# Optimization experiments

Measured on AMD Instinct MI355X. Metric: run time of the kernel, lower is better.

## Reference

```python
import jax, jax.numpy as jnp
import numpy as np

# -------- problem dimensions (match init_kwargs / input_specs) --------
B, N, D = 4, 16384, 64          # batch, nodes (=128*128 pixels), feature dim
Q = 128                         # plateau/propagation state width (hardcoded in forward)
W = H = 128                     # grid (hardcoded in forward)
E = 131072                      # edges per batch element
M = 4                           # num_masks = k_nodes - 1
NUM_ITERS = 25                  # GraphPropagator(num_iters=25)
ADJ_THRESH = 0.5                # GraphPropagator(adj_thresh=0.5)


def setup_inputs() -> dict:
    key = jax.random.key(0)
    k1, k2, k3, k4 = jax.random.split(key, 4)
    node_features = jax.random.normal(k1, (B, N, D), dtype=jnp.float32)
    # global node indices in [0, B*N) -- the torch code concatenates per-batch
    # edge lists directly into a (B*N, B*N) SparseTensor
    node_edges = jax.random.randint(k2, (B, 2, E), 0, B * N)
    node_weights = jax.random.uniform(k3, (B, E), dtype=jnp.float32)
    init_state = jax.random.normal(k4, (B, N, Q), dtype=jnp.float32)
    return {"node_features": node_features, "node_edges": node_edges,
            "node_weights": node_weights, "init_state": init_state}


def _propagate(init_state, rows, cols, ws):
    """25-iteration sparse label propagation on the global (B*N,B*N) graph."""
    h = init_state.reshape(B * N, Q)

    def step(h, _):
        msg = ws[:, None] * h[cols]                                  # gather  [B*E, Q]
        agg = jax.ops.segment_sum(msg, rows, num_segments=B * N)    # scatter [B*N, Q]
        hn = agg / (jnp.linalg.norm(agg, axis=-1, keepdims=True) + 1e-8)
        return hn, None

    h, _ = jax.lax.scan(step, h, None, length=NUM_ITERS)
    return h  # [B*N, Q]


def _competition(platmap):
    """Competition(num_masks=M): agents claim pixels by plateau-vector affinity;
    an extra zero-logit background channel yields the unharvested mask."""
    flat = platmap.reshape(B, W * H, Q)
    agent_idx = jnp.linspace(0, W * H - 1, M).astype(jnp.int32)      # deterministic agent pixels
    agents = flat[:, agent_idx, :]                                   # [B, M, Q]
    logits = jnp.einsum('bnq,bmq->bnm', flat, agents) / jnp.sqrt(jnp.float32(Q))
    logits_ext = jnp.concatenate([logits, jnp.zeros((B, W * H, 1), logits.dtype)], axis=-1)
    probs = jax.nn.softmax(logits_ext, axis=-1)                      # [B, WH, M+1]
    masks = probs[..., :M].reshape(B, W, H, M)
    unharv = probs[..., M:].reshape(B, W, H, 1)
    alive = jnp.ones((B, M, 1), dtype=platmap.dtype)
    pheno = agents
    return masks, agents, alive, pheno, unharv


def reference(node_features, node_edges, node_weights, init_state):
    rows = node_edges[:, 0, :].reshape(-1)                           # [B*E] global row idx
    cols = node_edges[:, 1, :].reshape(-1)
    ws = node_weights.reshape(-1)
    ws = jnp.where(ws > ADJ_THRESH, ws, jnp.float32(0.0))            # adjacency threshold

    prop = _propagate(init_state, rows, cols, ws)                    # [B*N, Q]
    platmap = prop.reshape(B, W, H, Q)

    masks, agents, alive, pheno, unharv = _competition(platmap)
    masks_ext = jnp.concatenate([masks, unharv], axis=-1)            # [B, W, H, M+1]
    masks_ext = jnp.transpose(masks_ext, (0, 3, 1, 2))               # [B, M+1, W, H]

    nf = jnp.einsum('bnd,bmn->bmd', node_features,
                    masks_ext.reshape(B, M + 1, W * H))              # [B, M+1, D]
    # F.normalize(p=2, dim=1, eps=1e-12)
    nf = nf / jnp.clip(jnp.linalg.norm(nf, axis=1, keepdims=True), 1e-12)
    node_scores = jnp.max(masks_ext, axis=(-1, -2))                  # [B, M+1]
    return nf, masks_ext, node_scores
```

## Files before the change

### kernel.cpp

```cpp
#include <hip/hip_runtime.h>

#define B_    4
#define N_    16384
#define D_    64
#define Q_    128
#define E_    131072
#define M_    4
#define BN    65536
#define TOTE  524288
#define ITERS 25
#define PAD_CAP (TOTE + 3 * BN + 64)

#define OFF_MASKS 1280
#define OFF_SCORES 328960

__constant__ int c_agidx[4] = {0, 5461, 10922, 16383};

__device__ __forceinline__ unsigned pack_bf16x2(float x, float y) {
    unsigned ux = __float_as_uint(x);
    unsigned uy = __float_as_uint(y);
    ux = (ux + 0x7fffu + ((ux >> 16) & 1u)) >> 16;
    uy = (uy + 0x7fffu + ((uy >> 16) & 1u)) & 0xffff0000u;
    return ux | uy;
}

__global__ void k_count(const int* __restrict__ edges, const float* __restrict__ wts,
                        int* __restrict__ deg) {
    int idx = blockIdx.x * blockDim.x + threadIdx.x;
    if (idx >= TOTE) return;
    int b = idx >> 17;
    int e = idx & (E_ - 1);
    float w = wts[idx];
    if (w > 0.5f) {
        int row = edges[(b * 2) * E_ + e];
        atomicAdd(&deg[row], 1);
    }
}

__global__ __launch_bounds__(256) void k_scan1(const int* __restrict__ deg,
                                               int* __restrict__ blockSums) {
    int i = blockIdx.x * 256 + threadIdx.x;
    int v = (deg[i] + 3) & ~3;
    #pragma unroll
    for (int off = 1; off < 64; off <<= 1) v += __shfl_xor(v, off, 64);
    __shared__ int ws[4];
    int lane = threadIdx.x & 63, w = threadIdx.x >> 6;
    if (lane == 0) ws[w] = v;
    __syncthreads();
    if (threadIdx.x == 0)
        blockSums[blockIdx.x] = ws[0] + ws[1] + ws[2] + ws[3];
}

__global__ __launch_bounds__(256) void k_scan2(const int* __restrict__ blockSums,
                                               int* __restrict__ blockOffs,
                                               int* __restrict__ row_start) {
    int t = threadIdx.x;
    int lane = t & 63, w = t >> 6;
    int v = blockSums[t];
    int incl = v;
    #pragma unroll
    for (int off = 1; off < 64; off <<= 1) {
        int u = __shfl_up(incl, off, 64);
        if (lane >= off) incl += u;
    }
    __shared__ int wtot[4];
    if (lane == 63) wtot[w] = incl;
    __syncthreads();
    int wadd = 0;
    for (int j = 0; j < w; ++j) wadd += wtot[j];
    incl += wadd;
    blockOffs[t] = incl - v;
    if (t == 255) row_start[BN] = incl;
}

__global__ __launch_bounds__(256) void k_scan3(const int* __restrict__ deg,
                                               const int* __restrict__ blockOffs,
                                               int* __restrict__ row_start,
                                               int* __restrict__ cursor) {
    int t = threadIdx.x;
    int lane = t & 63, w = t >> 6;
    int i = blockIdx.x * 256 + t;
    int v = (deg[i] + 3) & ~3;
    int incl = v;
    #pragma unroll
    for (int off = 1; off < 64; off <<= 1) {
        int u = __shfl_up(incl, off, 64);
        if (lane >= off) incl += u;
    }
    __shared__ int wtot[4];
    if (lane == 63) wtot[w] = incl;
    __syncthreads();
    int wadd = 0;
    for (int j = 0; j < w; ++j) wadd += wtot[j];
    int rs = blockOffs[blockIdx.x] + wadd + incl - v;
    row_start[i] = rs;
    cursor[i] = rs;
}

__global__ void k_scatter(const int* __restrict__ edges, const float* __restrict__ wts,
                          int* __restrict__ cursor, int2* __restrict__ cw) {
    int idx = blockIdx.x * blockDim.x + threadIdx.x;
    if (idx >= TOTE) return;
    int b = idx >> 17;
    int e = idx & (E_ - 1);
    float w = wts[idx];
    if (w > 0.5f) {
        int row = edges[(b * 2) * E_ + e];
        int col = edges[(b * 2) * E_ + E_ + e];
        int pos = atomicAdd(&cursor[row], 1);
        cw[pos] = make_int2(col, __float_as_int(w));
    }
}

__global__ void k_sort(const int* __restrict__ row_start, const int* __restrict__ deg,
                       int2* __restrict__ cw) {
    int n = blockIdx.x * blockDim.x + threadIdx.x;
    if (n >= BN) return;
    int s = row_start[n], epos = s + deg[n], pend = row_start[n + 1];
    for (int i = s + 1; i < epos; ++i) {
        int2 v = cw[i];
        unsigned long long key =
            ((unsigned long long)(unsigned)v.x << 32) | (unsigned)v.y;
        int j = i - 1;
        while (j >= s) {
            int2 u = cw[j];
            unsigned long long kj =
                ((unsigned long long)(unsigned)u.x << 32) | (unsigned)u.y;
            if (kj <= key) break;
            cw[j + 1] = u;
            --j;
        }
        cw[j + 1] = v;
    }
    for (int i = epos; i < pend; ++i) cw[i] = make_int2(0, 0);
}

template <bool F32IN>
__global__ __launch_bounds__(256) void k_prop(const void* __restrict__ hin,
                                              unsigned* __restrict__ hout,
                                              const int* __restrict__ row_start,
                                              const int2* __restrict__ cw) {
    int lane = threadIdx.x & 63;
    int node = (blockIdx.x << 2) + (threadIdx.x >> 6);
    int unode = __builtin_amdgcn_readfirstlane(node);
    int s = row_start[unode];
    int e = row_start[unode + 1];
    float ax = 0.f, ay = 0.f;

    auto gather = [&](int col) -> float2 {
        if constexpr (F32IN) {
            return ((const float2*)hin)[((size_t)col << 6) + lane];
        } else {
            unsigned p = ((const unsigned*)hin)[((size_t)col << 6) + lane];
            float2 r;
            r.x = __uint_as_float(p << 16);
            r.y = __uint_as_float(p & 0xffff0000u);
            return r;
        }
    };

    int i = s;
    for (; i + 8 <= e; i += 8) {
        const int4* q = (const int4*)(cw + i);
        int4 a = q[0];
        int4 b = q[1];
        int4 c = q[2];
        int4 d = q[3];
        float2 v0 = gather(a.x);
        float2 v1 = gather(a.z);
        float2 v2 = gather(b.x);
        float2 v3 = gather(b.z);
        float2 v4 = gather(c.x);
        float2 v5 = gather(c.z);
        float2 v6 = gather(d.x);
        float2 v7 = gather(d.z);
        float w0 = __int_as_float(a.y), w1 = __int_as_float(a.w);
        float w2 = __int_as_float(b.y), w3 = __int_as_float(b.w);
        float w4 = __int_as_float(c.y), w5 = __int_as_float(c.w);
        float w6 = __int_as_float(d.y), w7 = __int_as_float(d.w);
        ax = fmaf(w0, v0.x, ax); ay = fmaf(w0, v0.y, ay);
        ax = fmaf(w1, v1.x, ax); ay = fmaf(w1, v1.y, ay);
        ax = fmaf(w2, v2.x, ax); ay = fmaf(w2, v2.y, ay);
        ax = fmaf(w3, v3.x, ax); ay = fmaf(w3, v3.y, ay);
        ax = fmaf(w4, v4.x, ax); ay = fmaf(w4, v4.y, ay);
        ax = fmaf(w5, v5.x, ax); ay = fmaf(w5, v5.y, ay);
        ax = fmaf(w6, v6.x, ax); ay = fmaf(w6, v6.y, ay);
        ax = fmaf(w7, v7.x, ax); ay = fmaf(w7, v7.y, ay);
    }
    for (; i < e; i += 4) {
        const int4* q = (const int4*)(cw + i);
        int4 a = q[0];
        int4 b = q[1];
        float2 v0 = gather(a.x);
        float2 v1 = gather(a.z);
        float2 v2 = gather(b.x);
        float2 v3 = gather(b.z);
        float w0 = __int_as_float(a.y), w1 = __int_as_float(a.w);
        float w2 = __int_as_float(b.y), w3 = __int_as_float(b.w);
        ax = fmaf(w0, v0.x, ax); ay = fmaf(w0, v0.y, ay);
        ax = fmaf(w1, v1.x, ax); ay = fmaf(w1, v1.y, ay);
        ax = fmaf(w2, v2.x, ax); ay = fmaf(w2, v2.y, ay);
        ax = fmaf(w3, v3.x, ax); ay = fmaf(w3, v3.y, ay);
    }
    float ss = ax * ax + ay * ay;
    #pragma unroll
    for (int off = 32; off; off >>= 1) ss += __shfl_xor(ss, off, 64);
    float inv = 1.0f / (sqrtf(ss) + 1e-8f);
    hout[((size_t)unode << 6) + lane] = pack_bf16x2(ax * inv, ay * inv);
}

__global__ __launch_bounds__(256) void k_masks(const unsigned* __restrict__ h,
                                               float* __restrict__ masks) {
    int wave = threadIdx.x >> 6;
    int lane = threadIdx.x & 63;
    int n = blockIdx.x * 4 + wave;
    int b = n >> 14;
    int nl = n & (N_ - 1);
    unsigned vp = h[((size_t)n << 6) + lane];
    float vx = __uint_as_float(vp << 16);
    float vy = __uint_as_float(vp & 0xffff0000u);
    float dot[4];
    #pragma unroll
    for (int m = 0; m < 4; ++m) {
        int an = b * N_ + c_agidx[m];
        unsigned ap = h[((size_t)an << 6) + lane];
        float axx = __uint_as_float(ap << 16);
        float ayy = __uint_as_float(ap & 0xffff0000u);
        float d = vx * axx + vy * ayy;
        #pragma unroll
        for (int off = 32; off; off >>= 1) d += __shfl_xor(d, off, 64);
        dot[m] = d;
    }
    const float scl = 0.0883883476483184405501055452631f;
    float l0 = dot[0] * scl, l1 = dot[1] * scl, l2 = dot[2] * scl, l3 = dot[3] * scl;
    float mx = fmaxf(fmaxf(fmaxf(l0, l1), fmaxf(l2, l3)), 0.f);
    float e0 = expf(l0 - mx), e1 = expf(l1 - mx), e2 = expf(l2 - mx),
          e3 = expf(l3 - mx), e4 = expf(0.f - mx);
    float den = e0 + e1 + e2 + e3 + e4;
    if (lane < 5) {
        float p = (lane == 0) ? e0 : (lane == 1) ? e1 : (lane == 2) ? e2
                  : (lane == 3) ? e3 : e4;
        masks[((size_t)b * 5 + lane) * N_ + nl] = p / den;
    }
}

__global__ __launch_bounds__(256) void k_nfpart(const float* __restrict__ feat,
                                                const float* __restrict__ masks,
                                                float* __restrict__ part,
                                                float* __restrict__ maxpart) {
    int bm = blockIdx.x >> 6;
    int chunk = blockIdx.x & 63;
    int b = bm / 5;
    int d = threadIdx.x & 63;
    int g = threadIdx.x >> 6;
    int n0 = chunk * 256 + g * 64;
    const float* fb = feat + (size_t)b * N_ * D_;
    const float* mk = masks + (size_t)bm * N_;
    float acc = 0.f;
    float mxv = -1e30f;
    for (int i = 0; i < 64; ++i) {
        int n = n0 + i;
        float mv = mk[n];
        acc = fmaf(fb[(size_t)n * D_ + d], mv, acc);
        mxv = fmaxf(mxv, mv);
    }
    __shared__ float lds[4][64];
    __shared__ float lmx[4];
    lds[g][d] = acc;
    if (d == 0) lmx[g] = mxv;
    __syncthreads();
    if (g == 0) {
        float s = lds[0][d] + lds[1][d] + lds[2][d] + lds[3][d];
        part[(size_t)blockIdx.x * 64 + d] = s;
        if (d == 0)
            maxpart[blockIdx.x] = fmaxf(fmaxf(lmx[0], lmx[1]), fmaxf(lmx[2], lmx[3]));
    }
}

__global__ void k_nffinal(const float* __restrict__ part, const float* __restrict__ maxpart,
                          float* __restrict__ out) {
    int b = blockIdx.x;
    int d = threadIdx.x;
    float v[5];
    float ss = 0.f;
    for (int m = 0; m < 5; ++m) {
        int bm = b * 5 + m;
        float s = 0.f;
        for (int c = 0; c < 64; ++c) s += part[(size_t)(bm * 64 + c) * 64 + d];
        v[m] = s;
        ss += s * s;
    }
    float nrm = fmaxf(sqrtf(ss), 1e-12f);
    for (int m = 0; m < 5; ++m) out[((size_t)b * 5 + m) * 64 + d] = v[m] / nrm;
    if (d < 5) {
        int bm = b * 5 + d;
        float mx = -1e30f;
        for (int c = 0; c < 64; ++c) mx = fmaxf(mx, maxpart[bm * 64 + c]);
        out[OFF_SCORES + bm] = mx;
    }
}

extern "C" void kernel_launch(void* const* d_in, const int* in_sizes, int n_in,
                              void* d_out, int out_size, void* d_ws, size_t ws_size,
                              hipStream_t stream) {
    const float* feat  = (const float*)d_in[0];
    const int*   edges = (const int*)d_in[1];
    const float* wts   = (const float*)d_in[2];
    const float* init  = (const float*)d_in[3];
    float* out = (float*)d_out;

    unsigned* hA = (unsigned*)d_ws;
    unsigned* hB = hA + (size_t)BN * 64;
    int* row_start  = (int*)(hB + (size_t)BN * 64);
    int* cursor     = row_start + 65544;
    int* deg        = cursor + BN;
    int* blockSums  = deg + BN;
    int* blockOffs  = blockSums + 256;
    int2* cw        = (int2*)(blockOffs + 256);
    float* part     = (float*)(cw + PAD_CAP);
    float* maxpart  = part + 81920;

    hipMemsetAsync(deg, 0, BN * sizeof(int), stream);
    k_count<<<TOTE / 256, 256, 0, stream>>>(edges, wts, deg);
    k_scan1<<<256, 256, 0, stream>>>(deg, blockSums);
    k_scan2<<<1, 256, 0, stream>>>(blockSums, blockOffs, row_start);
    k_scan3<<<256, 256, 0, stream>>>(deg, blockOffs, row_start, cursor);
    k_scatter<<<TOTE / 256, 256, 0, stream>>>(edges, wts, cursor, cw);
    k_sort<<<BN / 256, 256, 0, stream>>>(row_start, deg, cw);

    k_prop<true><<<BN / 4, 256, 0, stream>>>(init, hA, row_start, cw);
    const unsigned* src = hA;
    for (int it = 1; it < ITERS; ++it) {
        unsigned* dst = (it & 1) ? hB : hA;
        k_prop<false><<<BN / 4, 256, 0, stream>>>(src, dst, row_start, cw);
        src = dst;
    }

    k_masks<<<BN / 4, 256, 0, stream>>>(src, out + OFF_MASKS);
    k_nfpart<<<20 * 64, 256, 0, stream>>>(feat, out + OFF_MASKS, part, maxpart);
    k_nffinal<<<4, 64, 0, stream>>>(part, maxpart, out);
}
```

Before: 554.8 us.

## Process two nodes per wavefront in propagation and fold scan2 into scan3

Each wavefront in the propagation kernel now handles two nodes, one in the lower half and one in the upper half of the node range. It walks both edge lists in lockstep, clamping indices and zeroing weights past each list's end. The goal is more gather loads in flight per wave and half as many waves. The cost is wasted gathers when the two degrees differ and some extra register pressure. The separate single-block scan2 kernel is removed: every scan3 block rescans all 256 block sums itself, which saves one launch at the price of redundant work.

```diff
diff --git a/kernel.cpp b/kernel.cpp
--- a/kernel.cpp
+++ b/kernel.cpp
@@ -51,34 +51,32 @@
         blockSums[blockIdx.x] = ws[0] + ws[1] + ws[2] + ws[3];
 }
 
-__global__ __launch_bounds__(256) void k_scan2(const int* __restrict__ blockSums,
-                                               int* __restrict__ blockOffs,
-                                               int* __restrict__ row_start) {
-    int t = threadIdx.x;
-    int lane = t & 63, w = t >> 6;
-    int v = blockSums[t];
-    int incl = v;
-    #pragma unroll
-    for (int off = 1; off < 64; off <<= 1) {
-        int u = __shfl_up(incl, off, 64);
-        if (lane >= off) incl += u;
-    }
-    __shared__ int wtot[4];
-    if (lane == 63) wtot[w] = incl;
-    __syncthreads();
-    int wadd = 0;
-    for (int j = 0; j < w; ++j) wadd += wtot[j];
-    incl += wadd;
-    blockOffs[t] = incl - v;
-    if (t == 255) row_start[BN] = incl;
-}
-
 __global__ __launch_bounds__(256) void k_scan3(const int* __restrict__ deg,
-                                               const int* __restrict__ blockOffs,
+                                               const int* __restrict__ blockSums,
                                                int* __restrict__ row_start,
                                                int* __restrict__ cursor) {
     int t = threadIdx.x;
     int lane = t & 63, w = t >> 6;
+    __shared__ int offs[256];
+    __shared__ int wtotA[4];
+    __shared__ int wtotB[4];
+
+    int bs = blockSums[t];
+    int binc = bs;
+    #pragma unroll
+    for (int off = 1; off < 64; off <<= 1) {
+        int u = __shfl_up(binc, off, 64);
+        if (lane >= off) binc += u;
+    }
+    if (lane == 63) wtotA[w] = binc;
+    __syncthreads();
+    int badd = 0;
+    for (int j = 0; j < w; ++j) badd += wtotA[j];
+    offs[t] = binc + badd - bs;
+    if (blockIdx.x == 0 && t == 255) row_start[BN] = binc + badd;
+    __syncthreads();
+    int blockOff = offs[blockIdx.x];
+
     int i = blockIdx.x * 256 + t;
     int v = (deg[i] + 3) & ~3;
     int incl = v;
@@ -87,12 +85,11 @@
         int u = __shfl_up(incl, off, 64);
         if (lane >= off) incl += u;
     }
-    __shared__ int wtot[4];
-    if (lane == 63) wtot[w] = incl;
+    if (lane == 63) wtotB[w] = incl;
     __syncthreads();
     int wadd = 0;
-    for (int j = 0; j < w; ++j) wadd += wtot[j];
-    int rs = blockOffs[blockIdx.x] + wadd + incl - v;
+    for (int j = 0; j < w; ++j) wadd += wtotB[j];
+    int rs = blockOff + wadd + incl - v;
     row_start[i] = rs;
     cursor[i] = rs;
 }
@@ -141,11 +138,17 @@
                                               const int* __restrict__ row_start,
                                               const int2* __restrict__ cw) {
     int lane = threadIdx.x & 63;
-    int node = (blockIdx.x << 2) + (threadIdx.x >> 6);
-    int unode = __builtin_amdgcn_readfirstlane(node);
-    int s = row_start[unode];
-    int e = row_start[unode + 1];
-    float ax = 0.f, ay = 0.f;
+    int gid = (blockIdx.x << 2) + (threadIdx.x >> 6);
+    int uA = __builtin_amdgcn_readfirstlane(gid);
+    int uB = uA + 32768;
+    int sA = row_start[uA], eA = row_start[uA + 1];
+    int sB = row_start[uB], eB = row_start[uB + 1];
+    int cA = (eA - sA) >> 2, cB = (eB - sB) >> 2;
+    int nmax = cA > cB ? cA : cB;
+    int baseA = cA ? sA : sB;
+    int baseB = cB ? sB : sA;
+    int lastA = (cA ? cA : 1) - 1;
+    int lastB = (cB ? cB : 1) - 1;
 
     auto gather = [&](int col) -> float2 {
         if constexpr (F32IN) {
@@ -159,54 +162,51 @@
         }
     };
 
-    int i = s;
-    for (; i + 8 <= e; i += 8) {
-        const int4* q = (const int4*)(cw + i);
-        int4 a = q[0];
-        int4 b = q[1];
-        int4 c = q[2];
-        int4 d = q[3];
-        float2 v0 = gather(a.x);
-        float2 v1 = gather(a.z);
-        float2 v2 = gather(b.x);
-        float2 v3 = gather(b.z);
-        float2 v4 = gather(c.x);
-        float2 v5 = gather(c.z);
-        float2 v6 = gather(d.x);
-        float2 v7 = gather(d.z);
-        float w0 = __int_as_float(a.y), w1 = __int_as_float(a.w);
-        float w2 = __int_as_float(b.y), w3 = __int_as_float(b.w);
-        float w4 = __int_as_float(c.y), w5 = __int_as_float(c.w);
-        float w6 = __int_as_float(d.y), w7 = __int_as_float(d.w);
-        ax = fmaf(w0, v0.x, ax); ay = fmaf(w0, v0.y, ay);
-        ax = fmaf(w1, v1.x, ax); ay = fmaf(w1, v1.y, ay);
-        ax = fmaf(w2, v2.x, ax); ay = fmaf(w2, v2.y, ay);
-        ax = fmaf(w3, v3.x, ax); ay = fmaf(w3, v3.y, ay);
-        ax = fmaf(w4, v4.x, ax); ay = fmaf(w4, v4.y, ay);
-        ax = fmaf(w5, v5.x, ax); ay = fmaf(w5, v5.y, ay);
-        ax = fmaf(w6, v6.x, ax); ay = fmaf(w6, v6.y, ay);
-        ax = fmaf(w7, v7.x, ax); ay = fmaf(w7, v7.y, ay);
-    }
-    for (; i < e; i += 4) {
-        const int4* q = (const int4*)(cw + i);
-        int4 a = q[0];
-        int4 b = q[1];
-        float2 v0 = gather(a.x);
-        float2 v1 = gather(a.z);
-        float2 v2 = gather(b.x);
-        float2 v3 = gather(b.z);
-        float w0 = __int_as_float(a.y), w1 = __int_as_float(a.w);
-        float w2 = __int_as_float(b.y), w3 = __int_as_float(b.w);
-        ax = fmaf(w0, v0.x, ax); ay = fmaf(w0, v0.y, ay);
-        ax = fmaf(w1, v1.x, ax); ay = fmaf(w1, v1.y, ay);
-        ax = fmaf(w2, v2.x, ax); ay = fmaf(w2, v2.y, ay);
-        ax = fmaf(w3, v3.x, ax); ay = fmaf(w3, v3.y, ay);
-    }
-    float ss = ax * ax + ay * ay;
-    #pragma unroll
-    for (int off = 32; off; off >>= 1) ss += __shfl_xor(ss, off, 64);
-    float inv = 1.0f / (sqrtf(ss) + 1e-8f);
-    hout[((size_t)unode << 6) + lane] = pack_bf16x2(ax * inv, ay * inv);
+    float axA = 0.f, ayA = 0.f, axB = 0.f, ayB = 0.f;
+    for (int j = 0; j < nmax; ++j) {
+        int jA = j < lastA ? j : lastA;
+        int jB = j < lastB ? j : lastB;
+        const int4* qA = (const int4*)(cw + baseA + (jA << 2));
+        const int4* qB = (const int4*)(cw + baseB + (jB << 2));
+        int4 a0 = qA[0], a1 = qA[1];
+        int4 b0 = qB[0], b1 = qB[1];
+        float2 vA0 = gather(a0.x);
+        float2 vA1 = gather(a0.z);
+        float2 vA2 = gather(a1.x);
+        float2 vA3 = gather(a1.z);
+        float2 vB0 = gather(b0.x);
+        float2 vB1 = gather(b0.z);
+        float2 vB2 = gather(b1.x);
+        float2 vB3 = gather(b1.z);
+        bool okA = j < cA, okB = j < cB;
+        float wA0 = okA ? __int_as_float(a0.y) : 0.f;
+        float wA1 = okA ? __int_as_float(a0.w) : 0.f;
+        float wA2 = okA ? __int_as_float(a1.y) : 0.f;
+        float wA3 = okA ? __int_as_float(a1.w) : 0.f;
+        float wB0 = okB ? __int_as_float(b0.y) : 0.f;
+        float wB1 = okB ? __int_as_float(b0.w) : 0.f;
+        float wB2 = okB ? __int_as_float(b1.y) : 0.f;
+        float wB3 = okB ? __int_as_float(b1.w) : 0.f;
+        axA = fmaf(wA0, vA0.x, axA); ayA = fmaf(wA0, vA0.y, ayA);
+        axA = fmaf(wA1, vA1.x, axA); ayA = fmaf(wA1, vA1.y, ayA);
+        axA = fmaf(wA2, vA2.x, axA); ayA = fmaf(wA2, vA2.y, ayA);
+        axA = fmaf(wA3, vA3.x, axA); ayA = fmaf(wA3, vA3.y, ayA);
+        axB = fmaf(wB0, vB0.x, axB); ayB = fmaf(wB0, vB0.y, ayB);
+        axB = fmaf(wB1, vB1.x, axB); ayB = fmaf(wB1, vB1.y, ayB);
+        axB = fmaf(wB2, vB2.x, axB); ayB = fmaf(wB2, vB2.y, ayB);
+        axB = fmaf(wB3, vB3.x, axB); ayB = fmaf(wB3, vB3.y, ayB);
+    }
+    float ssA = axA * axA + ayA * ayA;
+    float ssB = axB * axB + ayB * ayB;
+    #pragma unroll
+    for (int off = 32; off; off >>= 1) {
+        ssA += __shfl_xor(ssA, off, 64);
+        ssB += __shfl_xor(ssB, off, 64);
+    }
+    float invA = 1.0f / (sqrtf(ssA) + 1e-8f);
+    float invB = 1.0f / (sqrtf(ssB) + 1e-8f);
+    hout[((size_t)uA << 6) + lane] = pack_bf16x2(axA * invA, ayA * invA);
+    hout[((size_t)uB << 6) + lane] = pack_bf16x2(axB * invB, ayB * invB);
 }
 
 __global__ __launch_bounds__(256) void k_masks(const unsigned* __restrict__ h,
@@ -315,24 +315,22 @@
     int* cursor     = row_start + 65544;
     int* deg        = cursor + BN;
     int* blockSums  = deg + BN;
-    int* blockOffs  = blockSums + 256;
-    int2* cw        = (int2*)(blockOffs + 256);
+    int2* cw        = (int2*)(blockSums + 256);
     float* part     = (float*)(cw + PAD_CAP);
     float* maxpart  = part + 81920;
 
     hipMemsetAsync(deg, 0, BN * sizeof(int), stream);
     k_count<<<TOTE / 256, 256, 0, stream>>>(edges, wts, deg);
     k_scan1<<<256, 256, 0, stream>>>(deg, blockSums);
-    k_scan2<<<1, 256, 0, stream>>>(blockSums, blockOffs, row_start);
-    k_scan3<<<256, 256, 0, stream>>>(deg, blockOffs, row_start, cursor);
+    k_scan3<<<256, 256, 0, stream>>>(deg, blockSums, row_start, cursor);
     k_scatter<<<TOTE / 256, 256, 0, stream>>>(edges, wts, cursor, cw);
     k_sort<<<BN / 256, 256, 0, stream>>>(row_start, deg, cw);
 
-    k_prop<true><<<BN / 4, 256, 0, stream>>>(init, hA, row_start, cw);
+    k_prop<true><<<BN / 8, 256, 0, stream>>>(init, hA, row_start, cw);
     const unsigned* src = hA;
     for (int it = 1; it < ITERS; ++it) {
         unsigned* dst = (it & 1) ? hB : hA;
-        k_prop<false><<<BN / 4, 256, 0, stream>>>(src, dst, row_start, cw);
+        k_prop<false><<<BN / 8, 256, 0, stream>>>(src, dst, row_start, cw);
         src = dst;
     }
 
```

Result: faster. 506.9 us, median of 2 (-8.6%).
